# Optimization experiments

Hardware: AMD Instinct MI355X
Metric: run time of the kernel (lower is better)

## Reference

```python
import jax, jax.numpy as jnp
import numpy as np

B, N, K, C = 4, 4096, 32, 192  # batch, npoint, nsample, channels (C % 6 == 0)
EPS = 1e-5


def setup_inputs() -> dict:
    key = jax.random.key(0)
    ks = jax.random.split(key, 8)
    p = jax.random.normal(ks[0], (B, N, 3), jnp.float32)
    x = jax.random.normal(ks[1], (B, C, N), jnp.float32)
    idx = jax.random.randint(ks[2], (B, N, K), 0, N)  # ball-query neighbor ids
    W = jax.random.normal(ks[3], (C, C + 3), jnp.float32) * 0.05  # 1x1 conv weight
    gamma = 1.0 + 0.1 * jax.random.normal(ks[4], (C,), jnp.float32)
    beta = 0.1 * jax.random.normal(ks[5], (C,), jnp.float32)
    rmean = 0.1 * jax.random.normal(ks[6], (C,), jnp.float32)
    rvar = jax.random.uniform(ks[7], (C,), jnp.float32) + 0.5  # positive running var
    return dict(p=p, x=x, idx=idx, W=W, gamma=gamma, beta=beta, rmean=rmean, rvar=rvar)


def reference(p, x, idx, W, gamma, beta, rmean, rvar):
    # --- grouper: gather neighbors, relative coords ---
    pn = jax.vmap(lambda pp, ii: pp[ii])(p, idx)            # [B,N,K,3]
    dp = jnp.transpose(pn - p[:, :, None, :], (0, 3, 1, 2))  # [B,3,N,K]
    xj = jax.vmap(lambda xx, ii: xx[:, ii])(x, idx)          # [B,C,N,K]
    # --- PosPool sin/cos positional embedding fused with features ---
    feat_dim = C // 6
    dim_mat = jnp.power(500.0, jnp.arange(feat_dim, dtype=jnp.float32) / feat_dim)
    div = (50.0 * dp)[..., None] / dim_mat                   # [B,3,N,K,fd]
    pe = jnp.concatenate([jnp.sin(div), jnp.cos(div)], axis=-1)  # [B,3,N,K,2fd]
    pe = jnp.transpose(pe, (0, 1, 4, 2, 3)).reshape(B, C, N, K)  # [B,C,N,K]
    agg = xj * pe + pe
    # --- dp_fj concat -> 1x1 conv -> BN(eval) -> ReLU ---
    h = jnp.concatenate([dp, agg], axis=1)                   # [B,C+3,N,K]
    y = jnp.einsum('oc,bcnk->bonk', W, h)                    # [B,C,N,K]
    inv = gamma / jnp.sqrt(rvar + EPS)
    y = y * inv[:, None, None] + (beta - rmean * inv)[:, None, None]
    y = jax.nn.relu(y)
    # --- max reduction over neighbors ---
    return jnp.max(y, axis=-1)                               # [B,C,N]
```

## Files before the change

kernel.cpp:

```cpp
#include <hip/hip_runtime.h>
#include <math.h>

#define B_   4
#define N_   4096
#define K_   32
#define C_   192
#define CH_  195
#define KPAD 224
#define PTS  2
#define NKT  7
#define NNT  4
#define GRID ((B_ * N_) / PTS)

using half8 = __attribute__((ext_vector_type(8))) _Float16;
using f32x4 = __attribute__((ext_vector_type(4))) float;

__device__ _Float16 g_Wp[C_ * KPAD];
__device__ _Float16 g_xT[(size_t)B_ * N_ * C_];

__global__ __launch_bounds__(256) void prep_w(const float* __restrict__ W) {
    int i = blockIdx.x * 256 + threadIdx.x;
    if (i < C_ * KPAD) {
        int o = i / KPAD, r = i - o * KPAD;
        float v = 0.0f;
        if (r < 3)                  v = W[o * CH_ + r];
        else if (r >= 8 && r < 200) v = W[o * CH_ + 3 + (r - 8)];
        g_Wp[i] = (_Float16)v;
    }
}

__global__ __launch_bounds__(256) void prep_xt(const float* __restrict__ x) {
    __shared__ float s[64][193];
    const int tid = threadIdx.x;
    const int b   = blockIdx.y;
    const int n0  = blockIdx.x * 64;
#pragma unroll
    for (int i = 0; i < 12; ++i) {
        const int c = i * 16 + (tid >> 4);
        const int n = (tid & 15) * 4;
        const float4 v = *(const float4*)(x + ((size_t)b * C_ + c) * N_ + n0 + n);
        s[n + 0][c] = v.x; s[n + 1][c] = v.y; s[n + 2][c] = v.z; s[n + 3][c] = v.w;
    }
    __syncthreads();
    const int n = tid >> 2;
#pragma unroll
    for (int i = 0; i < 6; ++i) {
        const int ch = (tid & 3) + 4 * i;
        half8 v;
#pragma unroll
        for (int jj = 0; jj < 8; ++jj) v[jj] = (_Float16)s[n][ch * 8 + jj];
        *(half8*)(g_xT + ((size_t)b * N_ + n0 + n) * C_ + ch * 8) = v;
    }
}

__global__ __launch_bounds__(256, 4) void la_mfma(
    const float* __restrict__ p,
    const int*   __restrict__ idx,
    const float* __restrict__ gamma_,
    const float* __restrict__ beta_,
    const float* __restrict__ rmean,
    const float* __restrict__ rvar,
    float* __restrict__ out)
{
    __shared__ _Float16 hb[NKT * NNT * 64 * 8];
    __shared__ float s_inv[C_], s_bias[C_], s_invd[32];
    __shared__ float s_out[C_ * PTS];

    const int tid  = threadIdx.x;
    const int lane = tid & 63;
    const int w    = tid >> 6;

    const int q  = blockIdx.x & 7;
    const int sI = blockIdx.x >> 3;
    const int L  = q * (GRID / 8) + sI;
    const int bn0 = L * PTS;
    const int b   = bn0 >> 12;
    const int n0  = bn0 & (N_ - 1);

    if (tid < C_) {
        const float inv = gamma_[tid] * rsqrtf(rvar[tid] + 1e-5f);
        s_inv[tid]  = inv;
        s_bias[tid] = beta_[tid] - rmean[tid] * inv;
    }
    if (tid < 32) s_invd[tid] = exp2f(-(float)tid * 0.2801808715263400f);
    __syncthreads();

    {
        const int col = tid >> 2;
        const int q0  = tid & 3;
        const int nt  = col >> 4;
        const int lsl = col & 15;
        const int pt  = col >> 5;
        const int k   = col & 31;
        const int gp  = bn0 + pt;
        const int j   = idx[(size_t)gp * K_ + k];
        float d0 = p[(size_t)(b * N_ + j) * 3 + 0] - p[(size_t)gp * 3 + 0];
        float d1 = p[(size_t)(b * N_ + j) * 3 + 1] - p[(size_t)gp * 3 + 1];
        float d2 = p[(size_t)(b * N_ + j) * 3 + 2] - p[(size_t)gp * 3 + 2];
        const _Float16* xh = g_xT + ((size_t)b * N_ + j) * C_;

#pragma unroll
        for (int i = 0; i < 6; ++i) {
            const int chunk = q0 + 4 * i;
            const half8 v = *(const half8*)(xh + chunk * 8);
            half8 hv;
#pragma unroll
            for (int jj = 0; jj < 8; ++jj) {
                const int c = chunk * 8 + jj;
                const float dd = (c < 64) ? d0 : ((c < 128) ? d1 : d2);
                const float ang = 50.0f * dd * s_invd[c & 31]
                                + (((c & 63) < 32) ? 0.0f : 1.5707963f);
                const float pe = __sinf(ang);
                hv[jj] = (_Float16)(pe * ((float)v[jj] + 1.0f));
            }
            const int ro = chunk + 1;
            const int kt = ro >> 2, kq = ro & 3;
            *(half8*)(&hb[(size_t)((kt * NNT + nt) * 64 + kq * 16 + lsl) * 8]) = hv;
        }
        if (q0 == 0) {
            half8 hv = (half8)(_Float16)0.0f;
            hv[0] = (_Float16)d0; hv[1] = (_Float16)d1; hv[2] = (_Float16)d2;
            *(half8*)(&hb[(size_t)((0 * NNT + nt) * 64 + 0 * 16 + lsl) * 8]) = hv;
        } else {
            const int ro = 24 + q0;
            const int kt = ro >> 2, kq = ro & 3;
            *(half8*)(&hb[(size_t)((kt * NNT + nt) * 64 + kq * 16 + lsl) * 8]) = (half8)(_Float16)0.0f;
        }
    }
    __syncthreads();

    const int l15  = lane & 15;
    const int quad = lane >> 4;

    f32x4 acc[3][4];
#pragma unroll
    for (int i = 0; i < 3; ++i)
#pragma unroll
        for (int t = 0; t < 4; ++t) acc[i][t] = (f32x4)0.0f;

#pragma unroll
    for (int kt = 0; kt < 7; ++kt) {
        const int k0 = kt * 32 + quad * 8;
        half8 a[3], bf[4];
#pragma unroll
        for (int i = 0; i < 3; ++i) {
            const int m = (w * 3 + i) * 16 + l15;
            a[i] = *(const half8*)(g_Wp + (size_t)m * KPAD + k0);
        }
#pragma unroll
        for (int t = 0; t < 4; ++t)
            bf[t] = *(const half8*)(&hb[(size_t)((kt * NNT + t) * 64 + lane) * 8]);
#pragma unroll
        for (int i = 0; i < 3; ++i)
#pragma unroll
            for (int t = 0; t < 4; ++t)
                acc[i][t] = __builtin_amdgcn_mfma_f32_16x16x32_f16(a[i], bf[t], acc[i][t], 0, 0, 0);
    }

#pragma unroll
    for (int i = 0; i < 3; ++i) {
        const int mbase = (w * 3 + i) * 16 + quad * 4;
#pragma unroll
        for (int pt = 0; pt < PTS; ++pt) {
            const f32x4 va = acc[i][2 * pt];
            const f32x4 vb = acc[i][2 * pt + 1];
#pragma unroll
            for (int r = 0; r < 4; ++r) {
                const int m = mbase + r;
                const float inv = s_inv[m];
                const float bia = s_bias[m];
                float v = fmaxf(fmaf(va[r], inv, bia), fmaf(vb[r], inv, bia));
                v = fmaxf(v, __shfl_xor(v, 1));
                v = fmaxf(v, __shfl_xor(v, 2));
                v = fmaxf(v, __shfl_xor(v, 4));
                v = fmaxf(v, __shfl_xor(v, 8));
                if (l15 == 0) s_out[m * PTS + pt] = fmaxf(v, 0.0f);
            }
        }
    }
    __syncthreads();

    if (tid < C_) {
        const float2 o2 = *(const float2*)(&s_out[tid * PTS]);
        *(float2*)(&out[((size_t)b * C_ + tid) * N_ + n0]) = o2;
    }
}

extern "C" void kernel_launch(void* const* d_in, const int* in_sizes, int n_in,
                              void* d_out, int out_size, void* d_ws, size_t ws_size,
                              hipStream_t stream) {
    (void)in_sizes; (void)n_in; (void)out_size; (void)d_ws; (void)ws_size;
    const float* p      = (const float*)d_in[0];
    const float* x      = (const float*)d_in[1];
    const int*   idx    = (const int*)d_in[2];
    const float* W      = (const float*)d_in[3];
    const float* gamma_ = (const float*)d_in[4];
    const float* beta_  = (const float*)d_in[5];
    const float* rmean  = (const float*)d_in[6];
    const float* rvar   = (const float*)d_in[7];
    float* out = (float*)d_out;

    prep_w<<<(C_ * KPAD + 255) / 256, 256, 0, stream>>>(W);
    prep_xt<<<dim3(N_ / 64, B_), 256, 0, stream>>>(x);
    la_mfma<<<GRID, 256, 0, stream>>>(p, idx, gamma_, beta_, rmean, rvar, out);
}
```

Measured before the change: 174.9 us.

## Use hardware sin with folded scale, packed fp16 math, DPP reductions, smaller transpose tiles

The fused kernel now folds the 50/(2π) scale into a precomputed frequency table and calls the raw hardware sin (which takes revolutions), using a quarter-turn offset for cos. It also packs the pe*x+pe product into half2 arithmetic, remaps threads so each wave builds its own column tile, and replaces shuffle-based max reductions with DPP row ops. The output staging reuses the hb LDS buffer behind an extra barrier. The transpose prep kernel uses smaller 32x96 tiles to raise occupancy. Computing in fp16 and using raw hardware sin may reduce accuracy slightly.

```diff
diff --git a/kernel.cpp b/kernel.cpp
--- a/kernel.cpp
+++ b/kernel.cpp
@@ -12,11 +12,25 @@
 #define NNT  4
 #define GRID ((B_ * N_) / PTS)
 
-using half8 = __attribute__((ext_vector_type(8))) _Float16;
-using f32x4 = __attribute__((ext_vector_type(4))) float;
+using half8  = __attribute__((ext_vector_type(8))) _Float16;
+using half2v = __attribute__((ext_vector_type(2))) _Float16;
+using f32x4  = __attribute__((ext_vector_type(4))) float;
 
 __device__ _Float16 g_Wp[C_ * KPAD];
 __device__ _Float16 g_xT[(size_t)B_ * N_ * C_];
+
+__device__ __forceinline__ float dpp_max16(float v) {
+    int s;
+    s = __builtin_amdgcn_update_dpp(0, __float_as_int(v), 0xB1,  0xF, 0xF, true);
+    v = fmaxf(v, __int_as_float(s));
+    s = __builtin_amdgcn_update_dpp(0, __float_as_int(v), 0x4E,  0xF, 0xF, true);
+    v = fmaxf(v, __int_as_float(s));
+    s = __builtin_amdgcn_update_dpp(0, __float_as_int(v), 0x141, 0xF, 0xF, true);
+    v = fmaxf(v, __int_as_float(s));
+    s = __builtin_amdgcn_update_dpp(0, __float_as_int(v), 0x140, 0xF, 0xF, true);
+    v = fmaxf(v, __int_as_float(s));
+    return v;
+}
 
 __global__ __launch_bounds__(256) void prep_w(const float* __restrict__ W) {
     int i = blockIdx.x * 256 + threadIdx.x;
@@ -30,26 +44,30 @@
 }
 
 __global__ __launch_bounds__(256) void prep_xt(const float* __restrict__ x) {
-    __shared__ float s[64][193];
+    __shared__ float s[32][97];
     const int tid = threadIdx.x;
-    const int b   = blockIdx.y;
-    const int n0  = blockIdx.x * 64;
-#pragma unroll
-    for (int i = 0; i < 12; ++i) {
-        const int c = i * 16 + (tid >> 4);
-        const int n = (tid & 15) * 4;
-        const float4 v = *(const float4*)(x + ((size_t)b * C_ + c) * N_ + n0 + n);
-        s[n + 0][c] = v.x; s[n + 1][c] = v.y; s[n + 2][c] = v.z; s[n + 3][c] = v.w;
-    }
-    __syncthreads();
-    const int n = tid >> 2;
-#pragma unroll
-    for (int i = 0; i < 6; ++i) {
-        const int ch = (tid & 3) + 4 * i;
-        half8 v;
-#pragma unroll
-        for (int jj = 0; jj < 8; ++jj) v[jj] = (_Float16)s[n][ch * 8 + jj];
-        *(half8*)(g_xT + ((size_t)b * N_ + n0 + n) * C_ + ch * 8) = v;
+    const int b   = blockIdx.z;
+    const int c0  = blockIdx.y * 96;
+    const int n0  = blockIdx.x * 32;
+#pragma unroll
+    for (int it = 0; it < 3; ++it) {
+        const int c  = it * 32 + (tid >> 3);
+        const int n4 = (tid & 7) * 4;
+        const float4 v = *(const float4*)(x + ((size_t)b * C_ + c0 + c) * N_ + n0 + n4);
+        s[n4 + 0][c] = v.x; s[n4 + 1][c] = v.y; s[n4 + 2][c] = v.z; s[n4 + 3][c] = v.w;
+    }
+    __syncthreads();
+#pragma unroll
+    for (int it = 0; it < 2; ++it) {
+        const int t = it * 256 + tid;
+        if (t < 32 * 12) {
+            const int n  = t / 12;
+            const int ch = t - n * 12;
+            half8 v;
+#pragma unroll
+            for (int jj = 0; jj < 8; ++jj) v[jj] = (_Float16)s[n][ch * 8 + jj];
+            *(half8*)(g_xT + ((size_t)b * N_ + n0 + n) * C_ + c0 + ch * 8) = v;
+        }
     }
 }
 
@@ -63,8 +81,7 @@
     float* __restrict__ out)
 {
     __shared__ _Float16 hb[NKT * NNT * 64 * 8];
-    __shared__ float s_inv[C_], s_bias[C_], s_invd[32];
-    __shared__ float s_out[C_ * PTS];
+    __shared__ float s_inv[C_], s_bias[C_], s_fr[32];
 
     const int tid  = threadIdx.x;
     const int lane = tid & 63;
@@ -82,49 +99,54 @@
         s_inv[tid]  = inv;
         s_bias[tid] = beta_[tid] - rmean[tid] * inv;
     }
-    if (tid < 32) s_invd[tid] = exp2f(-(float)tid * 0.2801808715263400f);
+    if (tid < 32) s_fr[tid] = 7.9577471546e0f * exp2f(-(float)tid * 0.2801808715263400f);
     __syncthreads();
 
     {
-        const int col = tid >> 2;
-        const int q0  = tid & 3;
-        const int nt  = col >> 4;
-        const int lsl = col & 15;
+        const int lsl = lane & 15;
+        const int q0  = lane >> 4;
+        const int col = w * 16 + lsl;
         const int pt  = col >> 5;
         const int k   = col & 31;
         const int gp  = bn0 + pt;
         const int j   = idx[(size_t)gp * K_ + k];
-        float d0 = p[(size_t)(b * N_ + j) * 3 + 0] - p[(size_t)gp * 3 + 0];
-        float d1 = p[(size_t)(b * N_ + j) * 3 + 1] - p[(size_t)gp * 3 + 1];
-        float d2 = p[(size_t)(b * N_ + j) * 3 + 2] - p[(size_t)gp * 3 + 2];
+        const float d0 = p[(size_t)(b * N_ + j) * 3 + 0] - p[(size_t)gp * 3 + 0];
+        const float d1 = p[(size_t)(b * N_ + j) * 3 + 1] - p[(size_t)gp * 3 + 1];
+        const float d2 = p[(size_t)(b * N_ + j) * 3 + 2] - p[(size_t)gp * 3 + 2];
         const _Float16* xh = g_xT + ((size_t)b * N_ + j) * C_;
+
+        float sfr[8];
+#pragma unroll
+        for (int jj = 0; jj < 8; ++jj) sfr[jj] = s_fr[q0 * 8 + jj];
 
 #pragma unroll
         for (int i = 0; i < 6; ++i) {
             const int chunk = q0 + 4 * i;
             const half8 v = *(const half8*)(xh + chunk * 8);
+            const float dd  = (chunk < 8) ? d0 : ((chunk < 16) ? d1 : d2);
+            const float off = (chunk & 4) ? 0.25f : 0.0f;
             half8 hv;
 #pragma unroll
-            for (int jj = 0; jj < 8; ++jj) {
-                const int c = chunk * 8 + jj;
-                const float dd = (c < 64) ? d0 : ((c < 128) ? d1 : d2);
-                const float ang = 50.0f * dd * s_invd[c & 31]
-                                + (((c & 63) < 32) ? 0.0f : 1.5707963f);
-                const float pe = __sinf(ang);
-                hv[jj] = (_Float16)(pe * ((float)v[jj] + 1.0f));
+            for (int jj = 0; jj < 8; jj += 2) {
+                const float pe0 = __builtin_amdgcn_sinf(fmaf(dd, sfr[jj],     off));
+                const float pe1 = __builtin_amdgcn_sinf(fmaf(dd, sfr[jj + 1], off));
+                const half2v pe2 = __builtin_bit_cast(half2v, __builtin_amdgcn_cvt_pkrtz(pe0, pe1));
+                half2v v2; v2[0] = v[jj]; v2[1] = v[jj + 1];
+                const half2v r2 = pe2 * v2 + pe2;
+                hv[jj] = r2[0]; hv[jj + 1] = r2[1];
             }
             const int ro = chunk + 1;
             const int kt = ro >> 2, kq = ro & 3;
-            *(half8*)(&hb[(size_t)((kt * NNT + nt) * 64 + kq * 16 + lsl) * 8]) = hv;
+            *(half8*)(&hb[(size_t)((kt * NNT + w) * 64 + kq * 16 + lsl) * 8]) = hv;
         }
         if (q0 == 0) {
-            half8 hv = (half8)(_Float16)0.0f;
-            hv[0] = (_Float16)d0; hv[1] = (_Float16)d1; hv[2] = (_Float16)d2;
-            *(half8*)(&hb[(size_t)((0 * NNT + nt) * 64 + 0 * 16 + lsl) * 8]) = hv;
+            half8 hv0 = (half8)(_Float16)0.0f;
+            hv0[0] = (_Float16)d0; hv0[1] = (_Float16)d1; hv0[2] = (_Float16)d2;
+            *(half8*)(&hb[(size_t)((0 * NNT + w) * 64 + 0 * 16 + lsl) * 8]) = hv0;
         } else {
             const int ro = 24 + q0;
             const int kt = ro >> 2, kq = ro & 3;
-            *(half8*)(&hb[(size_t)((kt * NNT + nt) * 64 + kq * 16 + lsl) * 8]) = (half8)(_Float16)0.0f;
+            *(half8*)(&hb[(size_t)((kt * NNT + w) * 64 + kq * 16 + lsl) * 8]) = (half8)(_Float16)0.0f;
         }
     }
     __syncthreads();
@@ -156,6 +178,9 @@
             for (int t = 0; t < 4; ++t)
                 acc[i][t] = __builtin_amdgcn_mfma_f32_16x16x32_f16(a[i], bf[t], acc[i][t], 0, 0, 0);
     }
+
+    __syncthreads();
+    float* s_out = (float*)hb;
 
 #pragma unroll
     for (int i = 0; i < 3; ++i) {
@@ -170,10 +195,7 @@
                 const float inv = s_inv[m];
                 const float bia = s_bias[m];
                 float v = fmaxf(fmaf(va[r], inv, bia), fmaf(vb[r], inv, bia));
-                v = fmaxf(v, __shfl_xor(v, 1));
-                v = fmaxf(v, __shfl_xor(v, 2));
-                v = fmaxf(v, __shfl_xor(v, 4));
-                v = fmaxf(v, __shfl_xor(v, 8));
+                v = dpp_max16(v);
                 if (l15 == 0) s_out[m * PTS + pt] = fmaxf(v, 0.0f);
             }
         }
@@ -201,6 +223,6 @@
     float* out = (float*)d_out;
 
     prep_w<<<(C_ * KPAD + 255) / 256, 256, 0, stream>>>(W);
-    prep_xt<<<dim3(N_ / 64, B_), 256, 0, stream>>>(x);
+    prep_xt<<<dim3(N_ / 32, 2, B_), 256, 0, stream>>>(x);
     la_mfma<<<GRID, 256, 0, stream>>>(p, idx, gamma_, beta_, rmean, rvar, out);
 }
```

Result: no change. 173.0 us (-1.1%).
